# Kernel optimization log

Hardware: AMD Instinct MI355X
Metric: run time of the kernel (lower is better)

The kernel has to match this reference:

```python
import jax, jax.numpy as jnp
import numpy as np

T, D, E, K = 8192, 7168, 256, 8
G, LG = 8, 4  # n_expert_groups, n_limited_groups
ROUTE_SCALE = 2.5


def setup_inputs() -> dict:
    key = jax.random.key(0)
    k1, k2, k3 = jax.random.split(key, 3)
    x = jax.random.normal(k1, (T, D), dtype=jnp.float32)
    W = jax.random.normal(k2, (E, D), dtype=jnp.float32) * (1.0 / np.sqrt(D))
    bias = jax.random.normal(k3, (E,), dtype=jnp.float32) * 0.01
    return {"x": x, "W": W, "bias": bias}


def reference(x, W, bias):
    # linear scorer: [T, E]
    logits = jnp.einsum("td,ed->te", x, W)
    original_scores = jax.nn.sigmoid(logits)
    scores = original_scores + bias  # bias only affects routing, not weights

    # group selection: reshape [T, G, E//G]; group score = sum of top-2 (bias path)
    scores_g = scores.reshape(T, G, E // G)
    group_scores = jax.lax.top_k(scores_g, 2)[0].sum(axis=-1)  # [T, G]
    _, gidx = jax.lax.top_k(group_scores, LG)  # [T, LG]
    keep = jnp.any(jnp.arange(G)[None, None, :] == gidx[:, :, None], axis=1)  # [T, G]
    scores_masked = jnp.where(keep[:, :, None], scores_g, -jnp.inf).reshape(T, E)

    # final top-k experts
    _, indices = jax.lax.top_k(scores_masked, K)  # [T, K] int32
    weights = jnp.take_along_axis(original_scores, indices, axis=1)  # [T, K]
    weights = weights / weights.sum(axis=-1, keepdims=True)  # sigmoid normalization
    weights = weights * ROUTE_SCALE
    weights = weights.astype(x.dtype)

    # per-expert token counts (indices unique per row, so scatter(1)+sum == histogram)
    counts = jnp.zeros((E,), dtype=jnp.int32).at[indices.reshape(-1)].add(1)
    return weights, indices.astype(jnp.int64), counts
```

## Files before the change

kernel.cpp:

```cpp
#include <hip/hip_runtime.h>
#include <math.h>
#include <stdint.h>

#define T_TOK 8192
#define D_DIM 7168
#define E_EXP 256
#define K_SEL 8
#define G_GRP 8
#define LG_GRP 4
#define ROUTE_SCALE 2.5f

#define BM 128
#define BN 128
#define BK 64
#define NKT (D_DIM / BK)
#define SCALE_LO 2048.0f
#define INV_SCALE (1.0f / 2048.0f)

typedef _Float16 half_t;
typedef _Float16 half8 __attribute__((ext_vector_type(8)));
typedef float f32x4 __attribute__((ext_vector_type(4)));

#define WF_HALVES_PER_H (2 * 112 * 16 * 512)

__global__ __launch_bounds__(256)
void convert_W_kernel(const float* __restrict__ W, half_t* __restrict__ Wf) {
    const int u = blockIdx.x * 256 + threadIdx.x;
    const int slot = u & 63;
    const int ks   = (u >> 6) & 1;
    const int p    = (u >> 7) & 7;
    const int t2   = u >> 10;
    const int kt   = t2 % 112;
    const int nb   = t2 / 112;
    const int e = nb * 128 + p * 16 + (slot & 15);
    const int k = kt * 64 + ks * 32 + (slot >> 4) * 8;

    const float* src = W + (size_t)e * D_DIM + k;
    float4 v0 = *(const float4*)src;
    float4 v1 = *(const float4*)(src + 4);
    float f[8] = {v0.x, v0.y, v0.z, v0.w, v1.x, v1.y, v1.z, v1.w};
    half8 hi, lo;
    #pragma unroll
    for (int j = 0; j < 8; j++) {
        const half_t h = (half_t)f[j];
        hi[j] = h;
        lo[j] = (half_t)((f[j] - (float)h) * SCALE_LO);
    }
    *(half8*)&Wf[(size_t)u * 8] = hi;
    *(half8*)&Wf[(size_t)WF_HALVES_PER_H + (size_t)u * 8] = lo;
}

__global__ __launch_bounds__(256, 2)
void gemm_logits_f16split(const float* __restrict__ x,
                          const half_t* __restrict__ Wf,
                          float* __restrict__ planes,
                          int kt_len, int gshift) {
    __shared__ __align__(16) half_t Ah[8 * 2 * 64 * 8];
    __shared__ __align__(16) half_t Al[8 * 2 * 64 * 8];

    const int tid = threadIdx.x;
    const int bid = blockIdx.x;
    const int g     = bid & ((1 << gshift) - 1);
    const int j     = bid >> gshift;
    const int nb    = g & 1;
    const int split = g >> 1;
    const int row0 = j * BM;
    const int ks0  = split * kt_len;

    const float* __restrict__ xA = x + (size_t)row0 * D_DIM;
    float* __restrict__ plane = planes + (size_t)split * T_TOK * E_EXP;

    const int wave = tid >> 6, lane = tid & 63;
    const int q = lane >> 4;
    const int mp0 = (wave >> 1) * 4;
    const int np0 = (wave & 1) * 4;

    const half_t* __restrict__ wfh = Wf + ((size_t)nb * 112) * 16 * 512 + (size_t)lane * 8;
    const half_t* __restrict__ wfl = Wf + ((size_t)(2 + nb) * 112) * 16 * 512 + (size_t)lane * 8;

    float4 pa[4][2];

    auto load_A = [&](int kt) {
        const int kbase = kt * BK;
        #pragma unroll
        for (int i = 0; i < 4; i++) {
            const int u = i * 256 + tid;
            const int r = u >> 3, k8 = u & 7;
            const float* p = xA + (size_t)r * D_DIM + kbase + k8 * 8;
            pa[i][0] = *(const float4*)p;
            pa[i][1] = *(const float4*)(p + 4);
        }
    };

    auto stage_A = [&]() {
        #pragma unroll
        for (int i = 0; i < 4; i++) {
            const int u = i * 256 + tid;
            const int r = u >> 3, k8 = u & 7;
            float f[8] = {pa[i][0].x, pa[i][0].y, pa[i][0].z, pa[i][0].w,
                          pa[i][1].x, pa[i][1].y, pa[i][1].z, pa[i][1].w};
            half8 hi, lo;
            #pragma unroll
            for (int jj = 0; jj < 8; jj++) {
                const half_t h = (half_t)f[jj];
                hi[jj] = h;
                lo[jj] = (half_t)((f[jj] - (float)h) * SCALE_LO);
            }
            const int m = r & 15, qq = k8 & 3, kss = k8 >> 2;
            const int slot = (m + 16 * qq) ^ k8;
            const int off = (((r >> 4) * 2 + kss) * 64 + slot) * 8;
            *(half8*)&Ah[off] = hi;
            *(half8*)&Al[off] = lo;
        }
    };

    f32x4 ach[4][4] = {}, acc[4][4] = {};

    auto compute = [&](int kt, bool pref, int ktn) {
        half8 bh[4][2], bl[4][2];
        const size_t ktoff = (size_t)kt * (16 * 512);
        #pragma unroll
        for (int ni = 0; ni < 4; ni++)
            #pragma unroll
            for (int ks = 0; ks < 2; ks++) {
                const int s32 = (np0 + ni) * 2 + ks;
                bh[ni][ks] = *(const half8*)(wfh + ktoff + (size_t)s32 * 512);
                bl[ni][ks] = *(const half8*)(wfl + ktoff + (size_t)s32 * 512);
            }
        #pragma unroll
        for (int ks = 0; ks < 2; ks++) {
            const int slot = lane ^ ((ks << 2) | q);
            half8 ah[4], al[4];
            #pragma unroll
            for (int mi = 0; mi < 4; mi++) {
                const int off = (((mp0 + mi) * 2 + ks) * 64 + slot) * 8;
                ah[mi] = *(const half8*)&Ah[off];
                al[mi] = *(const half8*)&Al[off];
            }
            #pragma unroll
            for (int mi = 0; mi < 4; mi++)
                #pragma unroll
                for (int ni = 0; ni < 4; ni++) {
                    ach[mi][ni] = __builtin_amdgcn_mfma_f32_16x16x32_f16(ah[mi], bh[ni][ks], ach[mi][ni], 0, 0, 0);
                    acc[mi][ni] = __builtin_amdgcn_mfma_f32_16x16x32_f16(ah[mi], bl[ni][ks], acc[mi][ni], 0, 0, 0);
                    acc[mi][ni] = __builtin_amdgcn_mfma_f32_16x16x32_f16(al[mi], bh[ni][ks], acc[mi][ni], 0, 0, 0);
                }
            if (ks == 0 && pref) load_A(ktn);
        }
    };

    load_A(ks0);

    #pragma unroll 1
    for (int tt = 0; tt < kt_len; tt++) {
        __syncthreads();
        stage_A();
        __syncthreads();
        compute(ks0 + tt, tt + 1 < kt_len, ks0 + tt + 1);
    }

    const int col0 = nb * BN;
    #pragma unroll
    for (int mi = 0; mi < 4; mi++)
        #pragma unroll
        for (int ni = 0; ni < 4; ni++) {
            const f32x4 vh = ach[mi][ni];
            const f32x4 vc = acc[mi][ni];
            const int ex = col0 + (np0 + ni) * 16 + (lane & 15);
            #pragma unroll
            for (int r = 0; r < 4; r++) {
                const int tok = row0 + (mp0 + mi) * 16 + q * 4 + r;
                plane[(size_t)tok * E_EXP + ex] = vh[r] + vc[r] * INV_SCALE;
            }
        }
}

__global__ __launch_bounds__(256)
void routing_kernel(const float* __restrict__ planes,
                    const float* __restrict__ bias,
                    float* __restrict__ out_w,
                    float* __restrict__ out_i,
                    int nsplit) {
    const int wave = threadIdx.x >> 6;
    const int lane = threadIdx.x & 63;
    const int t    = blockIdx.x * 4 + wave;

    float lg[4] = {0.f, 0.f, 0.f, 0.f};
    for (int s = 0; s < nsplit; s++) {
        const float4 l = *(const float4*)(planes + (size_t)s * T_TOK * E_EXP +
                                          (size_t)t * E_EXP + lane * 4);
        lg[0] += l.x; lg[1] += l.y; lg[2] += l.z; lg[3] += l.w;
    }
    const float4 bi = *(const float4*)(bias + lane * 4);

    float orig[4], s[4];
    #pragma unroll
    for (int j = 0; j < 4; j++)
        orig[j] = 1.0f / (1.0f + expf(-lg[j]));
    s[0] = orig[0] + bi.x; s[1] = orig[1] + bi.y;
    s[2] = orig[2] + bi.z; s[3] = orig[3] + bi.w;

    float p1 = fmaxf(s[0], s[1]), p2 = fminf(s[0], s[1]);
    float q1 = fmaxf(s[2], s[3]), q2 = fminf(s[2], s[3]);
    float m1 = fmaxf(p1, q1);
    float m2 = fmaxf(fminf(p1, q1), (p1 >= q1) ? p2 : q2);

    #pragma unroll
    for (int off = 1; off <= 4; off <<= 1) {
        float o1 = __shfl_xor(m1, off);
        float o2 = __shfl_xor(m2, off);
        float M1 = fmaxf(m1, o1);
        float M2 = fmaxf(fminf(m1, o1), (m1 >= o1) ? m2 : o2);
        m1 = M1; m2 = M2;
    }
    const float gscore = m1 + m2;

    const int g = lane >> 3;
    int cnt = 0;
    #pragma unroll
    for (int j = 0; j < G_GRP; j++) {
        float gj = __shfl(gscore, j * 8);
        cnt += (gj > gscore || (gj == gscore && j < g)) ? 1 : 0;
    }
    const bool keep = (cnt < LG_GRP);

    float smask[4];
    #pragma unroll
    for (int j = 0; j < 4; j++) smask[j] = keep ? s[j] : -INFINITY;

    float wsum = 0.0f, my_o = 0.0f;
    int my_i = 0;

    #pragma unroll
    for (int k = 0; k < K_SEL; k++) {
        float bv = smask[0]; float bo = orig[0]; int bs = 0;
        if (smask[1] > bv) { bv = smask[1]; bo = orig[1]; bs = 1; }
        if (smask[2] > bv) { bv = smask[2]; bo = orig[2]; bs = 2; }
        if (smask[3] > bv) { bv = smask[3]; bo = orig[3]; bs = 3; }
        int bidx = lane * 4 + bs;

        #pragma unroll
        for (int off = 32; off >= 1; off >>= 1) {
            float ov = __shfl_xor(bv, off);
            float oo = __shfl_xor(bo, off);
            int   oi = __shfl_xor(bidx, off);
            if (ov > bv || (ov == bv && oi < bidx)) { bv = ov; bo = oo; bidx = oi; }
        }
        wsum += bo;
        if (lane == k) { my_o = bo; my_i = bidx; }
        if ((bidx >> 2) == lane) {
            const int sl = bidx & 3;
            smask[0] = (sl == 0) ? -INFINITY : smask[0];
            smask[1] = (sl == 1) ? -INFINITY : smask[1];
            smask[2] = (sl == 2) ? -INFINITY : smask[2];
            smask[3] = (sl == 3) ? -INFINITY : smask[3];
        }
    }

    if (lane < K_SEL) {
        out_w[(size_t)t * K_SEL + lane] = my_o * ROUTE_SCALE / wsum;
        out_i[(size_t)t * K_SEL + lane] = (float)my_i;
    }
}

__global__ __launch_bounds__(256)
void count_kernel(const float* __restrict__ idxf, float* __restrict__ out_c) {
    const float fe = (float)blockIdx.x;
    int c = 0;
    const float4* p = (const float4*)idxf;
    for (int i = threadIdx.x; i < (T_TOK * K_SEL / 4); i += 256) {
        float4 v = p[i];
        c += (v.x == fe) + (v.y == fe) + (v.z == fe) + (v.w == fe);
    }
    __shared__ int red[4];
    #pragma unroll
    for (int off = 32; off >= 1; off >>= 1) c += __shfl_down(c, off);
    if ((threadIdx.x & 63) == 0) red[threadIdx.x >> 6] = c;
    __syncthreads();
    if (threadIdx.x == 0)
        out_c[blockIdx.x] = (float)(red[0] + red[1] + red[2] + red[3]);
}

extern "C" void kernel_launch(void* const* d_in, const int* in_sizes, int n_in,
                              void* d_out, int out_size, void* d_ws, size_t ws_size,
                              hipStream_t stream) {
    const float* x    = (const float*)d_in[0];
    const float* W    = (const float*)d_in[1];
    const float* bias = (const float*)d_in[2];

    float* out   = (float*)d_out;
    float* out_w = out;
    float* out_i = out + (size_t)T_TOK * K_SEL;
    float* out_c = out + (size_t)2 * T_TOK * K_SEL;

    const size_t planeN  = (size_t)T_TOK * E_EXP;
    const size_t wfBytes = (size_t)2 * WF_HALVES_PER_H * sizeof(half_t);

    int nsplit = 4;
    if (ws_size != 0 && ws_size < 4 * planeN * sizeof(float) + wfBytes)
        nsplit = 2;
    const int gshift = (nsplit == 4) ? 3 : 2;
    const int kt_len = NKT / nsplit;
    const int grid   = 64 * 2 * nsplit;

    float* planes = (float*)d_ws;
    half_t* Wf    = (half_t*)(planes + (size_t)nsplit * planeN);

    hipLaunchKernelGGL(convert_W_kernel, dim3(896), dim3(256), 0, stream, W, Wf);
    hipLaunchKernelGGL(gemm_logits_f16split, dim3(grid), dim3(256), 0, stream,
                       x, Wf, planes, kt_len, gshift);
    hipLaunchKernelGGL(routing_kernel, dim3(T_TOK / 4), dim3(256), 0, stream,
                       planes, bias, out_w, out_i, nsplit);
    hipLaunchKernelGGL(count_kernel, dim3(E_EXP), dim3(256), 0, stream,
                       out_i, out_c);
}
```

Baseline: 415.0 us.

## Halve GEMM row tile, stage W-hi via async LDS loads, use three K-splits

The M tile shrinks from 128 to 64 rows and occupancy is raised to 3 blocks per CU. The high half of W is now double-buffered in shared memory through global_load_lds, where before each wave read it directly from global memory. The K split drops from 4 to 3 uneven chunks, which gives 768 blocks and fewer partial planes for the routing kernel to sum. The aims are better load balance across CUs and less global traffic for W-hi per wave. The costs are less reuse of A per block and more shared-memory use per block.

```diff
diff --git a/kernel.cpp b/kernel.cpp
--- a/kernel.cpp
+++ b/kernel.cpp
@@ -10,7 +10,7 @@
 #define LG_GRP 4
 #define ROUTE_SCALE 2.5f
 
-#define BM 128
+#define BM 64
 #define BN 128
 #define BK 64
 #define NKT (D_DIM / BK)
@@ -22,6 +22,12 @@
 typedef float f32x4 __attribute__((ext_vector_type(4)));
 
 #define WF_HALVES_PER_H (2 * 112 * 16 * 512)
+
+__device__ __forceinline__ void load_lds16(const void* g, void* l) {
+    __builtin_amdgcn_global_load_lds(
+        (const __attribute__((address_space(1))) uint32_t*)g,
+        (__attribute__((address_space(3))) uint32_t*)l, 16, 0, 0);
+}
 
 __global__ __launch_bounds__(256)
 void convert_W_kernel(const float* __restrict__ W, half_t* __restrict__ Wf) {
@@ -50,40 +56,47 @@
     *(half8*)&Wf[(size_t)WF_HALVES_PER_H + (size_t)u * 8] = lo;
 }
 
-__global__ __launch_bounds__(256, 2)
+__global__ __launch_bounds__(256, 3)
 void gemm_logits_f16split(const float* __restrict__ x,
                           const half_t* __restrict__ Wf,
                           float* __restrict__ planes,
-                          int kt_len, int gshift) {
-    __shared__ __align__(16) half_t Ah[8 * 2 * 64 * 8];
-    __shared__ __align__(16) half_t Al[8 * 2 * 64 * 8];
+                          int nsplit) {
+    __shared__ __align__(16) half_t Ah[4 * 2 * 64 * 8];
+    __shared__ __align__(16) half_t Al[4 * 2 * 64 * 8];
+    __shared__ __align__(16) half_t Bbuf[2][16][512];
 
     const int tid = threadIdx.x;
     const int bid = blockIdx.x;
-    const int g     = bid & ((1 << gshift) - 1);
-    const int j     = bid >> gshift;
+    const int nmod  = 2 * nsplit;
+    const int g     = bid % nmod;
+    const int j     = bid / nmod;
     const int nb    = g & 1;
     const int split = g >> 1;
     const int row0 = j * BM;
-    const int ks0  = split * kt_len;
+
+    int ks0, kt_len;
+    if (nsplit == 3) { ks0 = split * 38 - (split == 2 ? 1 : 0);
+                       kt_len = split ? 37 : 38; }
+    else             { ks0 = split * (NKT / nsplit);
+                       kt_len = NKT / nsplit; }
 
     const float* __restrict__ xA = x + (size_t)row0 * D_DIM;
     float* __restrict__ plane = planes + (size_t)split * T_TOK * E_EXP;
 
     const int wave = tid >> 6, lane = tid & 63;
     const int q = lane >> 4;
-    const int mp0 = (wave >> 1) * 4;
+    const int mp0 = (wave >> 1) * 2;
     const int np0 = (wave & 1) * 4;
 
-    const half_t* __restrict__ wfh = Wf + ((size_t)nb * 112) * 16 * 512 + (size_t)lane * 8;
-    const half_t* __restrict__ wfl = Wf + ((size_t)(2 + nb) * 112) * 16 * 512 + (size_t)lane * 8;
-
-    float4 pa[4][2];
+    const half_t* __restrict__ wfl = Wf + ((size_t)(2 + nb) * 112) * 16 * 512
+                                        + (size_t)lane * 8;
+
+    float4 pa[2][2];
 
     auto load_A = [&](int kt) {
         const int kbase = kt * BK;
         #pragma unroll
-        for (int i = 0; i < 4; i++) {
+        for (int i = 0; i < 2; i++) {
             const int u = i * 256 + tid;
             const int r = u >> 3, k8 = u & 7;
             const float* p = xA + (size_t)r * D_DIM + kbase + k8 * 8;
@@ -94,7 +107,7 @@
 
     auto stage_A = [&]() {
         #pragma unroll
-        for (int i = 0; i < 4; i++) {
+        for (int i = 0; i < 2; i++) {
             const int u = i * 256 + tid;
             const int r = u >> 3, k8 = u & 7;
             float f[8] = {pa[i][0].x, pa[i][0].y, pa[i][0].z, pa[i][0].w,
@@ -114,41 +127,64 @@
         }
     };
 
-    f32x4 ach[4][4] = {}, acc[4][4] = {};
-
-    auto compute = [&](int kt, bool pref, int ktn) {
-        half8 bh[4][2], bl[4][2];
+    auto issue_B = [&](int tt) {
+        const int kt = ks0 + tt;
+        half_t* bb = &Bbuf[tt & 1][0][0];
+        #pragma unroll
+        for (int i = 0; i < 4; i++) {
+            const int sl = i * 4 + wave;
+            const half_t* src = Wf +
+                ((size_t)(nb * 112 + kt) * 16 + sl) * 512 + lane * 8;
+            load_lds16(src, bb + sl * 512);
+        }
+    };
+
+    f32x4 ach[2][4] = {}, acc[2][4] = {};
+
+    auto compute = [&](int tt, bool pref) {
+        const int kt = ks0 + tt;
+        const half_t* bb = &Bbuf[tt & 1][0][0];
+
+        half8 bl[4][2];
         const size_t ktoff = (size_t)kt * (16 * 512);
         #pragma unroll
         for (int ni = 0; ni < 4; ni++)
             #pragma unroll
             for (int ks = 0; ks < 2; ks++) {
                 const int s32 = (np0 + ni) * 2 + ks;
-                bh[ni][ks] = *(const half8*)(wfh + ktoff + (size_t)s32 * 512);
                 bl[ni][ks] = *(const half8*)(wfl + ktoff + (size_t)s32 * 512);
             }
+        if (pref) {
+            issue_B(tt + 1);
+            load_A(ks0 + tt + 1);
+        }
         #pragma unroll
         for (int ks = 0; ks < 2; ks++) {
             const int slot = lane ^ ((ks << 2) | q);
-            half8 ah[4], al[4];
-            #pragma unroll
-            for (int mi = 0; mi < 4; mi++) {
+            half8 ah[2], al[2], bh[4];
+            #pragma unroll
+            for (int mi = 0; mi < 2; mi++) {
                 const int off = (((mp0 + mi) * 2 + ks) * 64 + slot) * 8;
                 ah[mi] = *(const half8*)&Ah[off];
                 al[mi] = *(const half8*)&Al[off];
             }
             #pragma unroll
-            for (int mi = 0; mi < 4; mi++)
+            for (int ni = 0; ni < 4; ni++) {
+                const int s32 = (np0 + ni) * 2 + ks;
+                bh[ni] = *(const half8*)&bb[s32 * 512 + lane * 8];
+            }
+            #pragma unroll
+            for (int mi = 0; mi < 2; mi++)
                 #pragma unroll
                 for (int ni = 0; ni < 4; ni++) {
-                    ach[mi][ni] = __builtin_amdgcn_mfma_f32_16x16x32_f16(ah[mi], bh[ni][ks], ach[mi][ni], 0, 0, 0);
+                    ach[mi][ni] = __builtin_amdgcn_mfma_f32_16x16x32_f16(ah[mi], bh[ni], ach[mi][ni], 0, 0, 0);
                     acc[mi][ni] = __builtin_amdgcn_mfma_f32_16x16x32_f16(ah[mi], bl[ni][ks], acc[mi][ni], 0, 0, 0);
-                    acc[mi][ni] = __builtin_amdgcn_mfma_f32_16x16x32_f16(al[mi], bh[ni][ks], acc[mi][ni], 0, 0, 0);
+                    acc[mi][ni] = __builtin_amdgcn_mfma_f32_16x16x32_f16(al[mi], bh[ni], acc[mi][ni], 0, 0, 0);
                 }
-            if (ks == 0 && pref) load_A(ktn);
         }
     };
 
+    issue_B(0);
     load_A(ks0);
 
     #pragma unroll 1
@@ -156,12 +192,12 @@
         __syncthreads();
         stage_A();
         __syncthreads();
-        compute(ks0 + tt, tt + 1 < kt_len, ks0 + tt + 1);
+        compute(tt, tt + 1 < kt_len);
     }
 
     const int col0 = nb * BN;
     #pragma unroll
-    for (int mi = 0; mi < 4; mi++)
+    for (int mi = 0; mi < 2; mi++)
         #pragma unroll
         for (int ni = 0; ni < 4; ni++) {
             const f32x4 vh = ach[mi][ni];
@@ -296,19 +332,17 @@
     const size_t planeN  = (size_t)T_TOK * E_EXP;
     const size_t wfBytes = (size_t)2 * WF_HALVES_PER_H * sizeof(half_t);
 
-    int nsplit = 4;
-    if (ws_size != 0 && ws_size < 4 * planeN * sizeof(float) + wfBytes)
+    int nsplit = 3;
+    if (ws_size != 0 && ws_size < 3 * planeN * sizeof(float) + wfBytes)
         nsplit = 2;
-    const int gshift = (nsplit == 4) ? 3 : 2;
-    const int kt_len = NKT / nsplit;
-    const int grid   = 64 * 2 * nsplit;
+    const int grid = 128 * 2 * nsplit;
 
     float* planes = (float*)d_ws;
     half_t* Wf    = (half_t*)(planes + (size_t)nsplit * planeN);
 
     hipLaunchKernelGGL(convert_W_kernel, dim3(896), dim3(256), 0, stream, W, Wf);
     hipLaunchKernelGGL(gemm_logits_f16split, dim3(grid), dim3(256), 0, stream,
-                       x, Wf, planes, kt_len, gshift);
+                       x, Wf, planes, nsplit);
     hipLaunchKernelGGL(routing_kernel, dim3(T_TOK / 4), dim3(256), 0, stream,
                        planes, bias, out_w, out_i, nsplit);
     hipLaunchKernelGGL(count_kernel, dim3(E_EXP), dim3(256), 0, stream,
```

After: 413.5 us. About the same (-0.4%).
